# Kernel tuning notes

Measured on AMD Instinct MI355X. Metric: run time of the kernel, lower is better.

## Reference

```python
import jax, jax.numpy as jnp
import numpy as np

B, G, T = 4096, 100, 24


def _greedy_dispatch(demand, caps, prices, slack_price):
    """Exact LP solution of: min prices@alloc + slack_price*slack
    s.t. 0<=alloc<=caps, sum(alloc)+slack = demand (per b,t).
    demand: [B,T] (nonneg), caps: [B,G,T], prices: [G], slack_price: scalar.
    Returns alloc [B,G,T], slack [B,T].
    """
    prices_all = jnp.concatenate([prices, slack_price[None]])        # [G+1]
    # slack capacity = demand itself (slack alone can absorb everything)
    caps_all = jnp.concatenate([caps, demand[:, None, :]], axis=1)    # [B,G+1,T]
    order = jnp.argsort(prices_all)                                   # merit order
    caps_s = caps_all[:, order, :]
    before = jnp.cumsum(caps_s, axis=1) - caps_s                      # capacity ahead in merit order
    alloc_s = jnp.clip(demand[:, None, :] - before, 0.0, caps_s)
    inv = jnp.argsort(order)
    alloc = alloc_s[:, inv, :]
    return alloc[:, :-1, :], alloc[:, -1, :]


def setup_inputs() -> dict:
    key = jax.random.key(0)
    k1, k2, k3, k4 = jax.random.split(key, 4)
    R_up = jax.random.uniform(k1, (B, G, T), dtype=jnp.float32)
    R_dn = jax.random.uniform(k2, (B, G, T), dtype=jnp.float32)
    omega_true = jax.random.normal(k3, (B, T), dtype=jnp.float32) * 5.0
    b_G = 10.0 + 40.0 * jax.random.uniform(k4, (G,), dtype=jnp.float32)  # marginal costs $/MWh
    return {
        "R_up": R_up,
        "R_dn": R_dn,
        "omega_true": omega_true,
        "b_G": b_G,
        "voll": jnp.float32(1000.0),
        "vosp": jnp.float32(500.0),
        "rt_up_ratio": jnp.float32(1.5),
        "rt_dn_ratio": jnp.float32(1.2),
    }


def reference(R_up, R_dn, omega_true, b_G, voll, vosp, rt_up_ratio, rt_dn_ratio):
    c_up = rt_up_ratio * b_G                                          # [G]
    c_dn = rt_dn_ratio * b_G                                          # [G]
    dem_up = jnp.maximum(omega_true, 0.0)                             # [B,T]
    dem_dn = jnp.maximum(-omega_true, 0.0)
    du, LS = _greedy_dispatch(dem_up, R_up, c_up, voll)
    dd, SP = _greedy_dispatch(dem_dn, R_dn, c_dn, vosp)
    rt_obj = (jnp.einsum('g,bgt->b', c_up, du)
              + jnp.einsum('g,bgt->b', c_dn, dd)
              + voll * LS.sum(axis=1) + vosp * SP.sum(axis=1))        # [B]
    return du, dd, LS, SP, rt_obj
```

## Files before the change

kernel.cpp:

```cpp
#include <hip/hip_runtime.h>

#define G_ 100
#define T_ 24
#define GP1 101
#define TILE (G_ * T_)
#define VPB (TILE / 4)
#define WPB 4
#define BLOCK (64 * WPB)

typedef float vfloat4 __attribute__((ext_vector_type(4)));

__global__ void setup_sort_kernel(const float* __restrict__ b_G,
                                  const float* __restrict__ voll,
                                  const float* __restrict__ vosp,
                                  const float* __restrict__ ru,
                                  const float* __restrict__ rd,
                                  int* __restrict__ order_out,
                                  float* __restrict__ price_out)
{
    __shared__ float pu[GP1], pd[GP1];
    int i = threadIdx.x;
    if (i < GP1) {
        if (i < G_) { float bg = b_G[i]; pu[i] = ru[0] * bg; pd[i] = rd[0] * bg; }
        else        { pu[i] = voll[0];   pd[i] = vosp[0]; }
    }
    __syncthreads();
    if (i < GP1) {
        float mu = pu[i], md = pd[i];
        int r0 = 0, r1 = 0;
        for (int j = 0; j < GP1; ++j) {
            float vu = pu[j], vd = pd[j];
            r0 += (vu < mu) || (vu == mu && j < i);
            r1 += (vd < md) || (vd == md && j < i);
        }
        order_out[r0] = i;        price_out[r0] = mu;
        order_out[GP1 + r1] = i;  price_out[GP1 + r1] = md;
    }
}

template<int N>
__device__ __forceinline__ void scan_chunk(int k0,
    const float* __restrict__ capp,
    const int* __restrict__ ordp, const float* __restrict__ prp,
    float* __restrict__ ldscol,
    float dem, float& before, float& objp)
{
    int gg[N]; float pr[N], cap[N];
#pragma unroll
    for (int j = 0; j < N; ++j) { gg[j] = ordp[k0 + j]; pr[j] = prp[k0 + j]; }
#pragma unroll
    for (int j = 0; j < N; ++j) cap[j] = capp[gg[j] * T_];
#pragma unroll
    for (int j = 0; j < N; ++j) {
        float a = fminf(fmaxf(dem - before, 0.f), cap[j]);
        before += cap[j];
        objp = fmaf(pr[j], a, objp);
        ldscol[gg[j] * T_] = a;
    }
}

__global__ __launch_bounds__(BLOCK, 4) void dispatch_kernel(
    const float* __restrict__ R_up, const float* __restrict__ R_dn,
    const float* __restrict__ omega,
    const int* __restrict__ ord_ws, const float* __restrict__ pr_ws,
    float* __restrict__ out, int B)
{
    __shared__ float s_tile[WPB * TILE];
    __shared__ float s_obj[WPB];

    const int tid  = threadIdx.x;
    const int w    = tid >> 6;
    const int lane = tid & 63;
    const int b = __builtin_amdgcn_readfirstlane(blockIdx.x * 2 + (w >> 1));
    const int p = __builtin_amdgcn_readfirstlane(w & 1);
    const size_t bgt = (size_t)B * TILE;
    float* __restrict__ tw = &s_tile[w * TILE];

#pragma unroll
    for (int j = 0; j < 9; ++j) *(vfloat4*)&tw[(lane + j * 64) * 4] = (vfloat4)(0.f);
    if (lane < VPB - 576)       *(vfloat4*)&tw[(lane + 576) * 4]    = (vfloat4)(0.f);

    const int t = (lane < T_) ? lane : 0;
    const int*   __restrict__ ordp = ord_ws + p * GP1;
    const float* __restrict__ prp  = pr_ws  + p * GP1;

    float objp = 0.f;
    if (lane < T_) {
        const float om  = omega[(size_t)b * T_ + t];
        const float dem = p ? fmaxf(-om, 0.f) : fmaxf(om, 0.f);
        const float* __restrict__ capp = (p ? R_dn : R_up) + (size_t)b * TILE + t;
        float* __restrict__ ldscol = tw + t;

        float before = 0.f;
        scan_chunk<16>( 0, capp, ordp, prp, ldscol, dem, before, objp);
        bool run = __any(before < dem);
        if (run) { scan_chunk<16>(16, capp, ordp, prp, ldscol, dem, before, objp);
                   run = __any(before < dem); }
        if (run) { scan_chunk< 8>(32, capp, ordp, prp, ldscol, dem, before, objp);
                   run = __any(before < dem); }
        if (run) { scan_chunk< 8>(40, capp, ordp, prp, ldscol, dem, before, objp);
                   run = __any(before < dem); }
        if (run) { scan_chunk< 8>(48, capp, ordp, prp, ldscol, dem, before, objp);
                   run = __any(before < dem); }
        if (run) { scan_chunk< 8>(56, capp, ordp, prp, ldscol, dem, before, objp);
                   run = __any(before < dem); }
        if (run) { scan_chunk< 8>(64, capp, ordp, prp, ldscol, dem, before, objp);
                   run = __any(before < dem); }
        if (run) { scan_chunk< 8>(72, capp, ordp, prp, ldscol, dem, before, objp);
                   run = __any(before < dem); }
        if (run) { scan_chunk< 8>(80, capp, ordp, prp, ldscol, dem, before, objp);
                   run = __any(before < dem); }
        if (run) { scan_chunk< 8>(88, capp, ordp, prp, ldscol, dem, before, objp);
                   run = __any(before < dem); }
        if (run)   scan_chunk< 4>(96, capp, ordp, prp, ldscol, dem, before, objp);

        float slackv = fmaxf(dem - before, 0.f);
        objp = fmaf(prp[GP1 - 1], slackv, objp);
        out[2 * bgt + (size_t)p * B * T_ + (size_t)b * T_ + t] = slackv;
    }

#pragma unroll
    for (int off = 32; off; off >>= 1) objp += __shfl_xor(objp, off, 64);
    if (lane == 0) s_obj[w] = objp;

    __builtin_amdgcn_wave_barrier();
    {
        vfloat4* __restrict__ dst = (vfloat4*)out + ((size_t)p * B + b) * VPB;
#pragma unroll
        for (int j = 0; j < 9; ++j)
            dst[lane + j * 64] = *(const vfloat4*)&tw[(lane + j * 64) * 4];
        if (lane < VPB - 576)
            dst[lane + 576] = *(const vfloat4*)&tw[(lane + 576) * 4];
    }

    __syncthreads();
    if (tid == 0)
        out[2 * bgt + 2 * (size_t)B * T_ + b] = s_obj[0] + s_obj[1];
    if (tid == 128)
        out[2 * bgt + 2 * (size_t)B * T_ + b] = s_obj[2] + s_obj[3];
}

extern "C" void kernel_launch(void* const* d_in, const int* in_sizes, int n_in,
                              void* d_out, int out_size, void* d_ws, size_t ws_size,
                              hipStream_t stream)
{
    const float* R_up  = (const float*)d_in[0];
    const float* R_dn  = (const float*)d_in[1];
    const float* omega = (const float*)d_in[2];
    const float* b_G   = (const float*)d_in[3];
    const float* voll  = (const float*)d_in[4];
    const float* vosp  = (const float*)d_in[5];
    const float* ru    = (const float*)d_in[6];
    const float* rd    = (const float*)d_in[7];

    const int B = in_sizes[0] / TILE;
    float* out = (float*)d_out;

    int*   ord_ws = (int*)d_ws;
    float* pr_ws  = (float*)((char*)d_ws + 2 * GP1 * sizeof(int));

    setup_sort_kernel<<<1, 128, 0, stream>>>(b_G, voll, vosp, ru, rd, ord_ws, pr_ws);

    dispatch_kernel<<<B / 2, BLOCK, 0, stream>>>(
        R_up, R_dn, omega, ord_ws, pr_ws, out, B);
}
```

Measured before the change: 151.4 us.

## Fuse merit-order sort into dispatch kernel and broadcast order via readlane

Removes the separate single-block sort kernel and launch. Every block now recomputes the rank-sort of the 101 prices in shared memory, then each wave keeps the order and price arrays in two registers per lane and fetches entries with readlane instead of global loads. This drops one kernel launch, the dependency between the two kernels, and the scalar/global loads inside the scan, but adds a redundant O(G^2) sort and two block barriers to each of the 2048 blocks.

```diff
diff --git a/kernel.cpp b/kernel.cpp
--- a/kernel.cpp
+++ b/kernel.cpp
@@ -10,44 +10,25 @@
 
 typedef float vfloat4 __attribute__((ext_vector_type(4)));
 
-__global__ void setup_sort_kernel(const float* __restrict__ b_G,
-                                  const float* __restrict__ voll,
-                                  const float* __restrict__ vosp,
-                                  const float* __restrict__ ru,
-                                  const float* __restrict__ rd,
-                                  int* __restrict__ order_out,
-                                  float* __restrict__ price_out)
-{
-    __shared__ float pu[GP1], pd[GP1];
-    int i = threadIdx.x;
-    if (i < GP1) {
-        if (i < G_) { float bg = b_G[i]; pu[i] = ru[0] * bg; pd[i] = rd[0] * bg; }
-        else        { pu[i] = voll[0];   pd[i] = vosp[0]; }
-    }
-    __syncthreads();
-    if (i < GP1) {
-        float mu = pu[i], md = pd[i];
-        int r0 = 0, r1 = 0;
-        for (int j = 0; j < GP1; ++j) {
-            float vu = pu[j], vd = pd[j];
-            r0 += (vu < mu) || (vu == mu && j < i);
-            r1 += (vd < md) || (vd == md && j < i);
-        }
-        order_out[r0] = i;        price_out[r0] = mu;
-        order_out[GP1 + r1] = i;  price_out[GP1 + r1] = md;
-    }
-}
-
 template<int N>
 __device__ __forceinline__ void scan_chunk(int k0,
     const float* __restrict__ capp,
-    const int* __restrict__ ordp, const float* __restrict__ prp,
+    int ord_lo, int ord_hi, float pr_lo, float pr_hi,
     float* __restrict__ ldscol,
     float dem, float& before, float& objp)
 {
     int gg[N]; float pr[N], cap[N];
 #pragma unroll
-    for (int j = 0; j < N; ++j) { gg[j] = ordp[k0 + j]; pr[j] = prp[k0 + j]; }
+    for (int j = 0; j < N; ++j) {
+        const int idx = k0 + j;
+        if (idx < 64) {
+            gg[j] = __builtin_amdgcn_readlane(ord_lo, idx);
+            pr[j] = __int_as_float(__builtin_amdgcn_readlane(__float_as_int(pr_lo), idx));
+        } else {
+            gg[j] = __builtin_amdgcn_readlane(ord_hi, idx - 64);
+            pr[j] = __int_as_float(__builtin_amdgcn_readlane(__float_as_int(pr_hi), idx - 64));
+        }
+    }
 #pragma unroll
     for (int j = 0; j < N; ++j) cap[j] = capp[gg[j] * T_];
 #pragma unroll
@@ -62,13 +43,36 @@
 __global__ __launch_bounds__(BLOCK, 4) void dispatch_kernel(
     const float* __restrict__ R_up, const float* __restrict__ R_dn,
     const float* __restrict__ omega,
-    const int* __restrict__ ord_ws, const float* __restrict__ pr_ws,
+    const float* __restrict__ b_G, const float* __restrict__ voll,
+    const float* __restrict__ vosp, const float* __restrict__ ru,
+    const float* __restrict__ rd,
     float* __restrict__ out, int B)
 {
     __shared__ float s_tile[WPB * TILE];
     __shared__ float s_obj[WPB];
 
     const int tid  = threadIdx.x;
+
+    if (tid < GP1) {
+        float mu, md;
+        if (tid < G_) { float bg = b_G[tid]; mu = ru[0] * bg; md = rd[0] * bg; }
+        else          { mu = voll[0];        md = vosp[0]; }
+        s_tile[tid] = mu; s_tile[128 + tid] = md;
+    }
+    __syncthreads();
+    if (tid < GP1) {
+        const float mu = s_tile[tid], md = s_tile[128 + tid];
+        int r0 = 0, r1 = 0;
+        for (int j = 0; j < GP1; ++j) {
+            float vu = s_tile[j], vd = s_tile[128 + j];
+            r0 += (vu < mu) || (vu == mu && j < tid);
+            r1 += (vd < md) || (vd == md && j < tid);
+        }
+        ((int*)s_tile)[256 + r0] = tid;  s_tile[512 + r0] = mu;
+        ((int*)s_tile)[384 + r1] = tid;  s_tile[640 + r1] = md;
+    }
+    __syncthreads();
+
     const int w    = tid >> 6;
     const int lane = tid & 63;
     const int b = __builtin_amdgcn_readfirstlane(blockIdx.x * 2 + (w >> 1));
@@ -76,13 +80,18 @@
     const size_t bgt = (size_t)B * TILE;
     float* __restrict__ tw = &s_tile[w * TILE];
 
+    const int hi_ok = (lane < GP1 - 64);
+    const int   ord_lo = ((const int*)s_tile)[256 + p * 128 + lane];
+    const int   ord_hi = hi_ok ? ((const int*)s_tile)[256 + p * 128 + 64 + lane] : 0;
+    const float pr_lo  = s_tile[512 + p * 128 + lane];
+    const float pr_hi  = hi_ok ? s_tile[512 + p * 128 + 64 + lane] : 0.f;
+    __syncthreads();
+
 #pragma unroll
     for (int j = 0; j < 9; ++j) *(vfloat4*)&tw[(lane + j * 64) * 4] = (vfloat4)(0.f);
     if (lane < VPB - 576)       *(vfloat4*)&tw[(lane + 576) * 4]    = (vfloat4)(0.f);
 
     const int t = (lane < T_) ? lane : 0;
-    const int*   __restrict__ ordp = ord_ws + p * GP1;
-    const float* __restrict__ prp  = pr_ws  + p * GP1;
 
     float objp = 0.f;
     if (lane < T_) {
@@ -92,30 +101,32 @@
         float* __restrict__ ldscol = tw + t;
 
         float before = 0.f;
-        scan_chunk<16>( 0, capp, ordp, prp, ldscol, dem, before, objp);
+        scan_chunk<16>( 0, capp, ord_lo, ord_hi, pr_lo, pr_hi, ldscol, dem, before, objp);
         bool run = __any(before < dem);
-        if (run) { scan_chunk<16>(16, capp, ordp, prp, ldscol, dem, before, objp);
+        if (run) { scan_chunk<16>(16, capp, ord_lo, ord_hi, pr_lo, pr_hi, ldscol, dem, before, objp);
                    run = __any(before < dem); }
-        if (run) { scan_chunk< 8>(32, capp, ordp, prp, ldscol, dem, before, objp);
+        if (run) { scan_chunk< 8>(32, capp, ord_lo, ord_hi, pr_lo, pr_hi, ldscol, dem, before, objp);
                    run = __any(before < dem); }
-        if (run) { scan_chunk< 8>(40, capp, ordp, prp, ldscol, dem, before, objp);
+        if (run) { scan_chunk< 8>(40, capp, ord_lo, ord_hi, pr_lo, pr_hi, ldscol, dem, before, objp);
                    run = __any(before < dem); }
-        if (run) { scan_chunk< 8>(48, capp, ordp, prp, ldscol, dem, before, objp);
+        if (run) { scan_chunk< 8>(48, capp, ord_lo, ord_hi, pr_lo, pr_hi, ldscol, dem, before, objp);
                    run = __any(before < dem); }
-        if (run) { scan_chunk< 8>(56, capp, ordp, prp, ldscol, dem, before, objp);
+        if (run) { scan_chunk< 8>(56, capp, ord_lo, ord_hi, pr_lo, pr_hi, ldscol, dem, before, objp);
                    run = __any(before < dem); }
-        if (run) { scan_chunk< 8>(64, capp, ordp, prp, ldscol, dem, before, objp);
+        if (run) { scan_chunk< 8>(64, capp, ord_lo, ord_hi, pr_lo, pr_hi, ldscol, dem, before, objp);
                    run = __any(before < dem); }
-        if (run) { scan_chunk< 8>(72, capp, ordp, prp, ldscol, dem, before, objp);
+        if (run) { scan_chunk< 8>(72, capp, ord_lo, ord_hi, pr_lo, pr_hi, ldscol, dem, before, objp);
                    run = __any(before < dem); }
-        if (run) { scan_chunk< 8>(80, capp, ordp, prp, ldscol, dem, before, objp);
+        if (run) { scan_chunk< 8>(80, capp, ord_lo, ord_hi, pr_lo, pr_hi, ldscol, dem, before, objp);
                    run = __any(before < dem); }
-        if (run) { scan_chunk< 8>(88, capp, ordp, prp, ldscol, dem, before, objp);
+        if (run) { scan_chunk< 8>(88, capp, ord_lo, ord_hi, pr_lo, pr_hi, ldscol, dem, before, objp);
                    run = __any(before < dem); }
-        if (run)   scan_chunk< 4>(96, capp, ordp, prp, ldscol, dem, before, objp);
+        if (run)   scan_chunk< 4>(96, capp, ord_lo, ord_hi, pr_lo, pr_hi, ldscol, dem, before, objp);
 
+        const float slack_pr =
+            __int_as_float(__builtin_amdgcn_readlane(__float_as_int(pr_hi), GP1 - 1 - 64));
         float slackv = fmaxf(dem - before, 0.f);
-        objp = fmaf(prp[GP1 - 1], slackv, objp);
+        objp = fmaf(slack_pr, slackv, objp);
         out[2 * bgt + (size_t)p * B * T_ + (size_t)b * T_ + t] = slackv;
     }
 
@@ -156,11 +167,6 @@
     const int B = in_sizes[0] / TILE;
     float* out = (float*)d_out;
 
-    int*   ord_ws = (int*)d_ws;
-    float* pr_ws  = (float*)((char*)d_ws + 2 * GP1 * sizeof(int));
-
-    setup_sort_kernel<<<1, 128, 0, stream>>>(b_G, voll, vosp, ru, rd, ord_ws, pr_ws);
-
     dispatch_kernel<<<B / 2, BLOCK, 0, stream>>>(
-        R_up, R_dn, omega, ord_ws, pr_ws, out, B);
+        R_up, R_dn, omega, b_G, voll, vosp, ru, rd, out, B);
 }
```

Measured after the change: 154.5 us. 2.0% more time.
